# Kernel optimization log

Measured on AMD Instinct MI355X. Metric: run time of the kernel, lower is better.

## Reference

```python
import jax, jax.numpy as jnp
import numpy as np

HIDDEN = 2048
NUM_HEADS = 16
NUM_KV_HEADS = 8
HEAD_DIM = 128
EPS = 1e-6
ROPE_THETA = 10000.0
SEQ = 2048
Q_SIZE = NUM_HEADS * HEAD_DIM
KV_SIZE = NUM_KV_HEADS * HEAD_DIM


def rmsnorm_f32(x, w, eps=EPS):
    # RMSNormF32: normalize in float32, scale by weight
    xf = x.astype(jnp.float32)
    var = jnp.mean(xf * xf, axis=-1, keepdims=True)
    return xf * jax.lax.rsqrt(var + eps) * w.astype(jnp.float32)


def apply_rope(x, cos, sin):
    # x: [S, H, D]; cos/sin: [S, D//2] (neox-style half split)
    half = x.shape[-1] // 2
    x1, x2 = x[..., :half], x[..., half:]
    c = cos[:, None, :]
    s = sin[:, None, :]
    return jnp.concatenate([x1 * c - x2 * s, x2 * c + x1 * s], axis=-1)


def setup_inputs() -> dict:
    key = jax.random.key(0)
    ks = jax.random.split(key, 6)
    return {
        "positions": jnp.arange(SEQ, dtype=jnp.int32),
        "hidden_states": jax.random.normal(ks[0], (SEQ, HIDDEN), jnp.float32),
        "ln_weight": 1.0 + 0.1 * jax.random.normal(ks[1], (HIDDEN,), jnp.float32),
        "qkv_weight": 0.02 * jax.random.normal(ks[2], (Q_SIZE + 2 * KV_SIZE, HIDDEN), jnp.float32),
        "q_norm_weight": 1.0 + 0.1 * jax.random.normal(ks[3], (HEAD_DIM,), jnp.float32),
        "k_norm_weight": 1.0 + 0.1 * jax.random.normal(ks[4], (HEAD_DIM,), jnp.float32),
        "o_weight": 0.02 * jax.random.normal(ks[5], (HIDDEN, Q_SIZE), jnp.float32),
    }


def reference(positions, hidden_states, ln_weight, qkv_weight, q_norm_weight, k_norm_weight, o_weight):
    S = hidden_states.shape[0]
    # 1. input RMSNorm (f32)
    normalized = rmsnorm_f32(hidden_states, ln_weight)
    # 2. fused QKV projection (no bias)
    qkv = normalized @ qkv_weight.T  # [S, q_size + 2*kv_size]
    q = qkv[:, :Q_SIZE].reshape(S, NUM_HEADS, HEAD_DIM)
    k = qkv[:, Q_SIZE:Q_SIZE + KV_SIZE].reshape(S, NUM_KV_HEADS, HEAD_DIM)
    v = qkv[:, Q_SIZE + KV_SIZE:].reshape(S, NUM_KV_HEADS, HEAD_DIM)
    # 3. RoPE (neox half-split, cache built from theta)
    inv_freq = ROPE_THETA ** (-jnp.arange(0, HEAD_DIM, 2, dtype=jnp.float32) / HEAD_DIM)
    freqs = positions.astype(jnp.float32)[:, None] * inv_freq[None, :]  # [S, D/2]
    cos, sin = jnp.cos(freqs), jnp.sin(freqs)
    q = apply_rope(q, cos, sin)
    k = apply_rope(k, cos, sin)
    # 4. per-head q/k RMSNorm (applied after RoPE, as in source)
    q = rmsnorm_f32(q, q_norm_weight)
    k = rmsnorm_f32(k, k_norm_weight)
    # 5. GQA expand kv heads
    rep = NUM_HEADS // NUM_KV_HEADS
    k = jnp.repeat(k, rep, axis=1)  # [S, NH, D]
    v = jnp.repeat(v, rep, axis=1)
    # 6. naive causal attention
    scores = jnp.einsum('shd,thd->hst', q, k) / (HEAD_DIM ** 0.5)  # [NH, S, S]
    causal = jnp.triu(jnp.ones((S, S), dtype=bool), k=1)
    scores = jnp.where(causal[None, :, :], -jnp.inf, scores)
    attn = jax.nn.softmax(scores, axis=-1)
    attn = jnp.nan_to_num(attn, nan=0.0)
    out = jnp.einsum('hst,thd->shd', attn, v).reshape(S, Q_SIZE)
    # 7. output projection
    return out @ o_weight.T
```

## Files before the change

### kernel.cpp

```cpp
#include <hip/hip_runtime.h>
#include <hip/hip_bf16.h>
#include <stdint.h>

typedef unsigned short u16;
typedef __attribute__((ext_vector_type(4))) float f32x4;
typedef __attribute__((ext_vector_type(8))) __bf16 bf16x8;
typedef __attribute__((ext_vector_type(8))) unsigned short u16x8;
typedef __attribute__((ext_vector_type(4))) unsigned short u16x4;

#define SEQ 2048
#define HID 2048
#define HD  128

__device__ __forceinline__ float b2f(u16 v) {
    union { float f; unsigned u; } c; c.u = ((unsigned)v) << 16; return c.f;
}
__device__ __forceinline__ u16 f2b(float f) {
    union { float f; unsigned u; } c; c.f = f;
    unsigned r = c.u + 0x7fffu + ((c.u >> 16) & 1u);
    return (u16)(r >> 16);
}
__device__ __forceinline__ bf16x8 tob(u16x8 v) {
    union { u16x8 u; bf16x8 b; } c; c.u = v; return c.b;
}
__device__ __forceinline__ u16x8 ld8(const u16* p) { return *(const u16x8*)p; }

typedef const __attribute__((address_space(1))) unsigned int* gas_ptr;
typedef __attribute__((address_space(3))) unsigned int* las_ptr;
__device__ __forceinline__ void gld16(const void* g, void* l) {
    __builtin_amdgcn_global_load_lds((gas_ptr)g, (las_ptr)l, 16, 0, 0);
}

__global__ __launch_bounds__(256) void k_conv(const float* __restrict__ src,
                                              u16* __restrict__ dst) {
    const size_t i = ((size_t)blockIdx.x * 256 + threadIdx.x) * 8;
    f32x4 a = *(const f32x4*)(src + i);
    f32x4 b = *(const f32x4*)(src + i + 4);
    u16x8 o;
#pragma unroll
    for (int e = 0; e < 4; ++e) { o[e] = f2b(a[e]); o[e + 4] = f2b(b[e]); }
    *(u16x8*)(dst + i) = o;
}

__global__ __launch_bounds__(256) void k_rmsnorm(const float* __restrict__ x,
                                                 const float* __restrict__ w,
                                                 u16* __restrict__ o) {
    const int row = blockIdx.x, t = threadIdx.x;
    const float* xr = x + (size_t)row * HID + t * 8;
    f32x4 xa = *(const f32x4*)xr;
    f32x4 xb = *(const f32x4*)(xr + 4);
    float xf[8]; float ss = 0.f;
#pragma unroll
    for (int e = 0; e < 4; ++e) { xf[e] = xa[e]; xf[e + 4] = xb[e]; }
#pragma unroll
    for (int e = 0; e < 8; ++e) ss += xf[e] * xf[e];
#pragma unroll
    for (int m = 32; m; m >>= 1) ss += __shfl_xor(ss, m);
    __shared__ float red[4];
    if ((t & 63) == 0) red[t >> 6] = ss;
    __syncthreads();
    ss = red[0] + red[1] + red[2] + red[3];
    const float sc = rsqrtf(ss * (1.0f / HID) + 1e-6f);
    f32x4 wa = *(const f32x4*)(w + t * 8);
    f32x4 wb = *(const f32x4*)(w + t * 8 + 4);
    u16x8 ov;
#pragma unroll
    for (int e = 0; e < 4; ++e) {
        ov[e] = f2b(xf[e] * sc * wa[e]);
        ov[e + 4] = f2b(xf[e + 4] * sc * wb[e]);
    }
    *(u16x8*)(o + (size_t)row * HID + t * 8) = ov;
}

#define STAGE_G(buf, k0)                                                      \
    do {                                                                      \
        char* a0 = (char*)&As[buf][0][0] + wave * 1024;                       \
        char* a1 = (char*)&As[buf][1][0] + wave * 1024;                       \
        char* b0 = (char*)&Bs[buf][0][0] + wave * 1024;                       \
        char* b1 = (char*)&Bs[buf][1][0] + wave * 1024;                       \
        gld16(ga + (k0), a0);                                                 \
        gld16(ga + (k0) + rowskip, a0 + 4096);                                \
        gld16(ga + (k0) + 32, a1);                                            \
        gld16(ga + (k0) + 32 + rowskip, a1 + 4096);                           \
        gld16(gb + (k0), b0);                                                 \
        gld16(gb + (k0) + rowskip, b0 + 4096);                                \
        gld16(gb + (k0) + 32, b1);                                            \
        gld16(gb + (k0) + 32 + rowskip, b1 + 4096);                           \
    } while (0)

__global__ __launch_bounds__(256) void k_gemm_qkv(const u16* __restrict__ A,
                                                  const u16* __restrict__ B,
                                                  u16* __restrict__ qraw,
                                                  u16* __restrict__ kraw,
                                                  u16* __restrict__ vtr,
                                                  int K) {
    __shared__ u16 As[2][2][128 * 32];
    __shared__ u16 Bs[2][2][128 * 32];
    const int tid = threadIdx.x;
    const int wave = tid >> 6, lane = tid & 63, quad = lane >> 4, l16 = lane & 15;
    const int wm = wave >> 1, wn = wave & 1;
    const int sw = (l16 >> 1) & 3;
    const int m0 = blockIdx.x * 128, n0 = blockIdx.y * 128;
    f32x4 acc[4][4];
#pragma unroll
    for (int i = 0; i < 4; ++i)
#pragma unroll
        for (int j = 0; j < 4; ++j) acc[i][j] = (f32x4){0.f, 0.f, 0.f, 0.f};

    const int gchunk = (tid & 3) ^ ((tid >> 3) & 3);
    const u16* ga = A + (size_t)(m0 + (tid >> 2)) * K + gchunk * 8;
    const u16* gb = B + (size_t)(n0 + (tid >> 2)) * K + gchunk * 8;
    const size_t rowskip = (size_t)64 * K;

    STAGE_G(0, 0);
    const int nk = K >> 6;
    for (int t = 0; t < nk; ++t) {
        const int cur = t & 1;
        if (t + 1 < nk) {
            STAGE_G(cur ^ 1, (t + 1) * 64);
            asm volatile("s_waitcnt vmcnt(8)" ::: "memory");
        } else {
            asm volatile("s_waitcnt vmcnt(0)" ::: "memory");
        }
        __builtin_amdgcn_s_barrier();
        asm volatile("" ::: "memory");
#pragma unroll
        for (int h = 0; h < 2; ++h) {
            const u16* as = &As[cur][h][0];
            const u16* bs = &Bs[cur][h][0];
            bf16x8 af[4], bfr[4];
#pragma unroll
            for (int i = 0; i < 4; ++i)
                af[i] = tob(ld8(as + (wm * 64 + i * 16 + l16) * 32 + ((quad ^ sw) << 3)));
#pragma unroll
            for (int j = 0; j < 4; ++j)
                bfr[j] = tob(ld8(bs + (wn * 64 + j * 16 + l16) * 32 + ((quad ^ sw) << 3)));
#pragma unroll
            for (int i = 0; i < 4; ++i)
#pragma unroll
                for (int j = 0; j < 4; ++j)
                    acc[i][j] = __builtin_amdgcn_mfma_f32_16x16x32_bf16(af[i], bfr[j], acc[i][j], 0, 0, 0);
        }
        asm volatile("" ::: "memory");
        __builtin_amdgcn_s_barrier();
    }
#pragma unroll
    for (int i = 0; i < 4; ++i) {
        const int row = m0 + wm * 64 + i * 16 + quad * 4;
#pragma unroll
        for (int j = 0; j < 4; ++j) {
            const int col = n0 + wn * 64 + j * 16 + l16;
#pragma unroll
            for (int r = 0; r < 4; ++r) {
                const u16 val = f2b(acc[i][j][r]);
                const int s = row + r;
                if (col < 2048) {
                    const int head = col >> 7, d = col & 127;
                    qraw[((size_t)head * SEQ + s) * HD + d] = val;
                } else if (col < 3072) {
                    const int c = col - 2048, kv = c >> 7, d = c & 127;
                    kraw[((size_t)kv * SEQ + s) * HD + d] = val;
                } else {
                    const int c = col - 3072, kv = c >> 7, d = c & 127;
                    vtr[(size_t)kv * HD * SEQ + (size_t)d * SEQ + s] = val;
                }
            }
        }
    }
}

__global__ __launch_bounds__(256) void k_gemm_of(const u16* __restrict__ A,
                                                 const u16* __restrict__ B,
                                                 float* __restrict__ C,
                                                 int N, int K) {
    __shared__ u16 As[2][2][128 * 32];
    __shared__ u16 Bs[2][2][128 * 32];
    const int tid = threadIdx.x;
    const int wave = tid >> 6, lane = tid & 63, quad = lane >> 4, l16 = lane & 15;
    const int wm = wave >> 1, wn = wave & 1;
    const int sw = (l16 >> 1) & 3;
    const int m0 = blockIdx.x * 128, n0 = blockIdx.y * 128;
    f32x4 acc[4][4];
#pragma unroll
    for (int i = 0; i < 4; ++i)
#pragma unroll
        for (int j = 0; j < 4; ++j) acc[i][j] = (f32x4){0.f, 0.f, 0.f, 0.f};

    const int gchunk = (tid & 3) ^ ((tid >> 3) & 3);
    const u16* ga = A + (size_t)(m0 + (tid >> 2)) * K + gchunk * 8;
    const u16* gb = B + (size_t)(n0 + (tid >> 2)) * K + gchunk * 8;
    const size_t rowskip = (size_t)64 * K;

    STAGE_G(0, 0);
    const int nk = K >> 6;
    for (int t = 0; t < nk; ++t) {
        const int cur = t & 1;
        if (t + 1 < nk) {
            STAGE_G(cur ^ 1, (t + 1) * 64);
            asm volatile("s_waitcnt vmcnt(8)" ::: "memory");
        } else {
            asm volatile("s_waitcnt vmcnt(0)" ::: "memory");
        }
        __builtin_amdgcn_s_barrier();
        asm volatile("" ::: "memory");
#pragma unroll
        for (int h = 0; h < 2; ++h) {
            const u16* as = &As[cur][h][0];
            const u16* bs = &Bs[cur][h][0];
            bf16x8 af[4], bfr[4];
#pragma unroll
            for (int i = 0; i < 4; ++i)
                af[i] = tob(ld8(as + (wm * 64 + i * 16 + l16) * 32 + ((quad ^ sw) << 3)));
#pragma unroll
            for (int j = 0; j < 4; ++j)
                bfr[j] = tob(ld8(bs + (wn * 64 + j * 16 + l16) * 32 + ((quad ^ sw) << 3)));
#pragma unroll
            for (int i = 0; i < 4; ++i)
#pragma unroll
                for (int j = 0; j < 4; ++j)
                    acc[i][j] = __builtin_amdgcn_mfma_f32_16x16x32_bf16(af[i], bfr[j], acc[i][j], 0, 0, 0);
        }
        asm volatile("" ::: "memory");
        __builtin_amdgcn_s_barrier();
    }
#pragma unroll
    for (int i = 0; i < 4; ++i) {
        const int row = m0 + wm * 64 + i * 16 + quad * 4;
#pragma unroll
        for (int j = 0; j < 4; ++j) {
            const int col = n0 + wn * 64 + j * 16 + l16;
#pragma unroll
            for (int r = 0; r < 4; ++r)
                C[(size_t)(row + r) * N + col] = acc[i][j][r];
        }
    }
}

__global__ __launch_bounds__(256) void k_ropenorm(const int* __restrict__ pos,
                                                  const float* __restrict__ qw,
                                                  const float* __restrict__ kw,
                                                  u16* __restrict__ qraw,
                                                  u16* __restrict__ kraw) {
    const int s = blockIdx.x;
    const int h = blockIdx.y * 4 + (threadIdx.x >> 6);
    const int d = threadIdx.x & 63;
    const bool isq = h < 16;
    u16* row = isq ? (qraw + ((size_t)h * SEQ + s) * HD)
                   : (kraw + ((size_t)(h - 16) * SEQ + s) * HD);
    const float x1 = b2f(row[d]), x2 = b2f(row[d + 64]);
    const float p = (float)pos[s];
    const float inv = exp2f(-(float)d * (2.0f / 128.0f) * 13.287712379549449f);
    const float fr = p * inv;
    const float c = cosf(fr), sn = sinf(fr);
    const float o1 = x1 * c - x2 * sn;
    const float o2 = x2 * c + x1 * sn;
    float ss = o1 * o1 + o2 * o2;
#pragma unroll
    for (int m = 32; m; m >>= 1) ss += __shfl_xor(ss, m);
    const float sc = rsqrtf(ss * (1.0f / HD) + 1e-6f);
    const float* w = isq ? qw : kw;
    row[d] = f2b(o1 * sc * w[d]);
    row[d + 64] = f2b(o2 * sc * w[d + 64]);
}

__global__ __launch_bounds__(256) void k_attn(const u16* __restrict__ qh,
                                              const u16* __restrict__ kh,
                                              const u16* __restrict__ vt,
                                              u16* __restrict__ out) {
    const int tid = threadIdx.x;
    const int wave = tid >> 6, lane = tid & 63, quad = lane >> 4, l16 = lane & 15;
    const int head = blockIdx.y;
    const int bx = blockIdx.x;
    const int f = (bx & 1) ? 31 - (bx >> 1) : (bx >> 1);
    const int qt = (head < 8) ? f : 31 - f;
    const int kvh = head >> 1;
    const int q0 = qt * 64;

    __shared__ u16 Ks[2][64 * 128];
    __shared__ u16 Vts[2][128 * 64];
    __shared__ u16 Ps[4][16 * 64];

    const u16* qbase = qh + ((size_t)head * SEQ + q0 + wave * 16) * HD;
    bf16x8 aq[4];
#pragma unroll
    for (int kk = 0; kk < 4; ++kk)
        aq[kk] = tob(ld8(qbase + l16 * HD + kk * 32 + quad * 8));

    f32x4 acco[8];
#pragma unroll
    for (int j = 0; j < 8; ++j) acco[j] = (f32x4){0.f, 0.f, 0.f, 0.f};
    float lsum = 0.f;

    const float sc = 0.08838834764831845f;
    const u16* kbase = kh + (size_t)kvh * SEQ * HD;
    const u16* vbase = vt + (size_t)kvh * HD * SEQ;
    const int ntiles = qt + 1;
    u16* pw = &Ps[wave][0];
    const int qrow_g = q0 + wave * 16 + l16;

    const u16* kg0 = kbase + (size_t)tid * 8;
    const u16* vg0 = vbase + (size_t)(tid >> 3) * SEQ + (size_t)(tid & 7) * 8;
    int kst[4], vst[4];
#pragma unroll
    for (int r = 0; r < 4; ++r) {
        const int krow = r * 16 + (tid >> 4);
        kst[r] = krow * 128 + (((tid & 15) ^ (krow & 7)) << 3);
        const int vrow = r * 32 + (tid >> 3);
        vst[r] = vrow * 64 + (((tid & 7) ^ (vrow & 7)) << 3);
    }

    u16x8 kreg[4], vreg[4];
#pragma unroll
    for (int r = 0; r < 4; ++r) {
        kreg[r] = ld8(kg0 + (size_t)r * 2048);
        vreg[r] = ld8(vg0 + (size_t)r * 32 * SEQ);
    }
#pragma unroll
    for (int r = 0; r < 4; ++r) {
        *(u16x8*)(&Ks[0][0] + kst[r]) = kreg[r];
        *(u16x8*)(&Vts[0][0] + vst[r]) = vreg[r];
    }
    __syncthreads();

    for (int kt = 0; kt < ntiles; ++kt) {
        const int cur = kt & 1;
        const u16* ksc = &Ks[cur][0];
        const u16* vsc = &Vts[cur][0];

        if (kt + 1 < ntiles) {
            const size_t koff = (size_t)(kt + 1) * 64;
#pragma unroll
            for (int r = 0; r < 4; ++r) {
                kreg[r] = ld8(kg0 + koff * HD + (size_t)r * 2048);
                vreg[r] = ld8(vg0 + koff + (size_t)r * 32 * SEQ);
            }
        }

        f32x4 accs[4];
#pragma unroll
        for (int j = 0; j < 4; ++j) accs[j] = (f32x4){0.f, 0.f, 0.f, 0.f};
#pragma unroll
        for (int kk = 0; kk < 4; ++kk) {
#pragma unroll
            for (int j = 0; j < 4; ++j) {
                const int krow = j * 16 + l16;
                const bf16x8 bk = tob(ld8(ksc + krow * 128 + (((kk * 4 + quad) ^ (krow & 7)) << 3)));
                accs[j] = __builtin_amdgcn_mfma_f32_16x16x32_bf16(bk, aq[kk], accs[j], 0, 0, 0);
            }
        }

        const int k0 = kt * 64;
#pragma unroll
        for (int j = 0; j < 4; ++j) {
            u16x4 pk;
#pragma unroll
            for (int r = 0; r < 4; ++r) {
                const int kpos = k0 + j * 16 + quad * 4 + r;
                const float p = (kpos > qrow_g) ? 0.f : __expf(accs[j][r] * sc);
                lsum += p;
                pk[r] = f2b(p);
            }
            const int blk = (j * 2 + (quad >> 1)) ^ (l16 & 7);
            *(u16x4*)(pw + l16 * 64 + (blk << 3) + ((quad & 1) << 2)) = pk;
        }

        if (kt + 1 < ntiles) {
            u16* ksn = &Ks[1 - cur][0];
            u16* vsn = &Vts[1 - cur][0];
#pragma unroll
            for (int r = 0; r < 4; ++r) {
                *(u16x8*)(ksn + kst[r]) = kreg[r];
                *(u16x8*)(vsn + vst[r]) = vreg[r];
            }
        }

#pragma unroll
        for (int kk = 0; kk < 2; ++kk) {
            const bf16x8 ap = tob(ld8(pw + l16 * 64 + (((kk * 4 + quad) ^ (l16 & 7)) << 3)));
#pragma unroll
            for (int j = 0; j < 8; ++j) {
                const int vrow = j * 16 + l16;
                const bf16x8 bv = tob(ld8(vsc + vrow * 64 + (((kk * 4 + quad) ^ (vrow & 7)) << 3)));
                acco[j] = __builtin_amdgcn_mfma_f32_16x16x32_bf16(ap, bv, acco[j], 0, 0, 0);
            }
        }

        __syncthreads();
    }

    float v = lsum;
    v += __shfl_xor(v, 16);
    v += __shfl_xor(v, 32);
    f32x4 il;
#pragma unroll
    for (int r = 0; r < 4; ++r) il[r] = 1.0f / __shfl(v, quad * 4 + r);
    const int rowb = q0 + wave * 16 + quad * 4;
#pragma unroll
    for (int j = 0; j < 8; ++j) {
        const int col = head * HD + j * 16 + l16;
#pragma unroll
        for (int r = 0; r < 4; ++r)
            out[(size_t)(rowb + r) * 2048 + col] = f2b(acco[j][r] * il[r]);
    }
}

extern "C" void kernel_launch(void* const* d_in, const int* in_sizes, int n_in,
                              void* d_out, int out_size, void* d_ws, size_t ws_size,
                              hipStream_t stream) {
    const int*   positions = (const int*)d_in[0];
    const float* hidden   = (const float*)d_in[1];
    const float* lnw      = (const float*)d_in[2];
    const float* qkvw     = (const float*)d_in[3];
    const float* qnw      = (const float*)d_in[4];
    const float* knw      = (const float*)d_in[5];
    const float* ow       = (const float*)d_in[6];
    float* outp = (float*)d_out;

    char* ws = (char*)d_ws;
    const size_t MB = 1024ull * 1024ull;
    u16* normed = (u16*)(ws + 0 * MB);
    u16* qraw   = (u16*)(ws + 8 * MB);
    u16* kraw   = (u16*)(ws + 16 * MB);
    u16* vtr    = (u16*)(ws + 20 * MB);
    u16* qkvwb  = (u16*)(ws + 24 * MB);
    u16* owb    = (u16*)(ws + 0 * MB);
    u16* attno  = (u16*)(ws + 24 * MB);

    k_rmsnorm <<<SEQ, 256, 0, stream>>>(hidden, lnw, normed);
    k_conv    <<<4096, 256, 0, stream>>>(qkvw, qkvwb);
    k_gemm_qkv<<<dim3(16, 32), 256, 0, stream>>>(normed, qkvwb, qraw, kraw, vtr, HID);
    k_ropenorm<<<dim3(SEQ, 6), 256, 0, stream>>>(positions, qnw, knw, qraw, kraw);
    k_conv    <<<2048, 256, 0, stream>>>(ow, owb);
    k_attn    <<<dim3(32, 16), 256, 0, stream>>>(qraw, kraw, vtr, attno);
    k_gemm_of <<<dim3(16, 16), 256, 0, stream>>>(attno, owb, outp, HID, HID);
}
```

Before: 256.1 us.

## Split attention KV tiles across two wave groups with shared-memory reduction

```diff
diff --git a/kernel.cpp b/kernel.cpp
--- a/kernel.cpp
+++ b/kernel.cpp
@@ -263,12 +263,15 @@
     row[d + 64] = f2b(o2 * sc * w[d + 64]);
 }
 
-__global__ __launch_bounds__(256) void k_attn(const u16* __restrict__ qh,
-                                              const u16* __restrict__ kh,
-                                              const u16* __restrict__ vt,
-                                              u16* __restrict__ out) {
+__global__ __launch_bounds__(512, 4) void k_attn(const u16* __restrict__ qh,
+                                                 const u16* __restrict__ kh,
+                                                 const u16* __restrict__ vt,
+                                                 u16* __restrict__ out) {
     const int tid = threadIdx.x;
     const int wave = tid >> 6, lane = tid & 63, quad = lane >> 4, l16 = lane & 15;
+    const int gid = wave >> 2;
+    const int wv = wave & 3;
+    const int gtid = tid & 255;
     const int head = blockIdx.y;
     const int bx = blockIdx.x;
     const int f = (bx & 1) ? 31 - (bx >> 1) : (bx >> 1);
@@ -278,9 +281,9 @@
 
     __shared__ u16 Ks[2][64 * 128];
     __shared__ u16 Vts[2][128 * 64];
-    __shared__ u16 Ps[4][16 * 64];
-
-    const u16* qbase = qh + ((size_t)head * SEQ + q0 + wave * 16) * HD;
+    __shared__ u16 Ps[8][16 * 64];
+
+    const u16* qbase = qh + ((size_t)head * SEQ + q0 + wv * 16) * HD;
     bf16x8 aq[4];
 #pragma unroll
     for (int kk = 0; kk < 4; ++kk)
@@ -295,40 +298,46 @@
     const u16* kbase = kh + (size_t)kvh * SEQ * HD;
     const u16* vbase = vt + (size_t)kvh * HD * SEQ;
     const int ntiles = qt + 1;
+    const int niter = (ntiles + 1) >> 1;
     u16* pw = &Ps[wave][0];
-    const int qrow_g = q0 + wave * 16 + l16;
-
-    const u16* kg0 = kbase + (size_t)tid * 8;
-    const u16* vg0 = vbase + (size_t)(tid >> 3) * SEQ + (size_t)(tid & 7) * 8;
+    const int qrow_g = q0 + wv * 16 + l16;
+
+    const u16* kg0 = kbase + (size_t)gtid * 8;
+    const u16* vg0 = vbase + (size_t)(gtid >> 3) * SEQ + (size_t)(gtid & 7) * 8;
     int kst[4], vst[4];
 #pragma unroll
     for (int r = 0; r < 4; ++r) {
-        const int krow = r * 16 + (tid >> 4);
-        kst[r] = krow * 128 + (((tid & 15) ^ (krow & 7)) << 3);
-        const int vrow = r * 32 + (tid >> 3);
-        vst[r] = vrow * 64 + (((tid & 7) ^ (vrow & 7)) << 3);
-    }
+        const int krow = r * 16 + (gtid >> 4);
+        kst[r] = krow * 128 + (((gtid & 15) ^ (krow & 7)) << 3);
+        const int vrow = r * 32 + (gtid >> 3);
+        vst[r] = vrow * 64 + (((gtid & 7) ^ (vrow & 7)) << 3);
+    }
+    u16* ksg = &Ks[gid][0];
+    u16* vsg = &Vts[gid][0];
 
     u16x8 kreg[4], vreg[4];
-#pragma unroll
-    for (int r = 0; r < 4; ++r) {
-        kreg[r] = ld8(kg0 + (size_t)r * 2048);
-        vreg[r] = ld8(vg0 + (size_t)r * 32 * SEQ);
-    }
-#pragma unroll
-    for (int r = 0; r < 4; ++r) {
-        *(u16x8*)(&Ks[0][0] + kst[r]) = kreg[r];
-        *(u16x8*)(&Vts[0][0] + vst[r]) = vreg[r];
+    {
+        const size_t koff = (size_t)gid * 64;
+#pragma unroll
+        for (int r = 0; r < 4; ++r) {
+            kreg[r] = ld8(kg0 + koff * HD + (size_t)r * 2048);
+            vreg[r] = ld8(vg0 + koff + (size_t)r * 32 * SEQ);
+        }
+#pragma unroll
+        for (int r = 0; r < 4; ++r) {
+            *(u16x8*)(ksg + kst[r]) = kreg[r];
+            *(u16x8*)(vsg + vst[r]) = vreg[r];
+        }
     }
     __syncthreads();
 
-    for (int kt = 0; kt < ntiles; ++kt) {
-        const int cur = kt & 1;
-        const u16* ksc = &Ks[cur][0];
-        const u16* vsc = &Vts[cur][0];
-
-        if (kt + 1 < ntiles) {
-            const size_t koff = (size_t)(kt + 1) * 64;
+    for (int i = 0; i < niter; ++i) {
+        const int kt = 2 * i + gid;
+        const bool active = kt < ntiles;
+        const bool havenext = (kt + 2) < ntiles;
+
+        if (havenext) {
+            const size_t koff = (size_t)(kt + 2) * 64;
 #pragma unroll
             for (int r = 0; r < 4; ++r) {
                 kreg[r] = ld8(kg0 + koff * HD + (size_t)r * 2048);
@@ -336,71 +345,89 @@
             }
         }
 
-        f32x4 accs[4];
-#pragma unroll
-        for (int j = 0; j < 4; ++j) accs[j] = (f32x4){0.f, 0.f, 0.f, 0.f};
-#pragma unroll
-        for (int kk = 0; kk < 4; ++kk) {
+        if (active) {
+            f32x4 accs[4];
+#pragma unroll
+            for (int j = 0; j < 4; ++j) accs[j] = (f32x4){0.f, 0.f, 0.f, 0.f};
+#pragma unroll
+            for (int kk = 0; kk < 4; ++kk) {
+#pragma unroll
+                for (int j = 0; j < 4; ++j) {
+                    const int krow = j * 16 + l16;
+                    const bf16x8 bk = tob(ld8(ksg + krow * 128 + (((kk * 4 + quad) ^ (krow & 7)) << 3)));
+                    accs[j] = __builtin_amdgcn_mfma_f32_16x16x32_bf16(bk, aq[kk], accs[j], 0, 0, 0);
+                }
+            }
+
+            const int k0 = kt * 64;
 #pragma unroll
             for (int j = 0; j < 4; ++j) {
-                const int krow = j * 16 + l16;
-                const bf16x8 bk = tob(ld8(ksc + krow * 128 + (((kk * 4 + quad) ^ (krow & 7)) << 3)));
-                accs[j] = __builtin_amdgcn_mfma_f32_16x16x32_bf16(bk, aq[kk], accs[j], 0, 0, 0);
-            }
-        }
-
-        const int k0 = kt * 64;
-#pragma unroll
-        for (int j = 0; j < 4; ++j) {
-            u16x4 pk;
+                u16x4 pk;
+#pragma unroll
+                for (int r = 0; r < 4; ++r) {
+                    const int kpos = k0 + j * 16 + quad * 4 + r;
+                    const float p = (kpos > qrow_g) ? 0.f : __expf(accs[j][r] * sc);
+                    lsum += p;
+                    pk[r] = f2b(p);
+                }
+                const int blk = (j * 2 + (quad >> 1)) ^ (l16 & 7);
+                *(u16x4*)(pw + l16 * 64 + (blk << 3) + ((quad & 1) << 2)) = pk;
+            }
+
+#pragma unroll
+            for (int kk = 0; kk < 2; ++kk) {
+                const bf16x8 ap = tob(ld8(pw + l16 * 64 + (((kk * 4 + quad) ^ (l16 & 7)) << 3)));
+#pragma unroll
+                for (int j = 0; j < 8; ++j) {
+                    const int vrow = j * 16 + l16;
+                    const bf16x8 bv = tob(ld8(vsg + vrow * 64 + (((kk * 4 + quad) ^ (vrow & 7)) << 3)));
+                    acco[j] = __builtin_amdgcn_mfma_f32_16x16x32_bf16(ap, bv, acco[j], 0, 0, 0);
+                }
+            }
+        }
+
+        __syncthreads();
+        if (havenext) {
 #pragma unroll
             for (int r = 0; r < 4; ++r) {
-                const int kpos = k0 + j * 16 + quad * 4 + r;
-                const float p = (kpos > qrow_g) ? 0.f : __expf(accs[j][r] * sc);
-                lsum += p;
-                pk[r] = f2b(p);
-            }
-            const int blk = (j * 2 + (quad >> 1)) ^ (l16 & 7);
-            *(u16x4*)(pw + l16 * 64 + (blk << 3) + ((quad & 1) << 2)) = pk;
-        }
-
-        if (kt + 1 < ntiles) {
-            u16* ksn = &Ks[1 - cur][0];
-            u16* vsn = &Vts[1 - cur][0];
-#pragma unroll
-            for (int r = 0; r < 4; ++r) {
-                *(u16x8*)(ksn + kst[r]) = kreg[r];
-                *(u16x8*)(vsn + vst[r]) = vreg[r];
-            }
-        }
-
-#pragma unroll
-        for (int kk = 0; kk < 2; ++kk) {
-            const bf16x8 ap = tob(ld8(pw + l16 * 64 + (((kk * 4 + quad) ^ (l16 & 7)) << 3)));
-#pragma unroll
-            for (int j = 0; j < 8; ++j) {
-                const int vrow = j * 16 + l16;
-                const bf16x8 bv = tob(ld8(vsc + vrow * 64 + (((kk * 4 + quad) ^ (vrow & 7)) << 3)));
-                acco[j] = __builtin_amdgcn_mfma_f32_16x16x32_bf16(ap, bv, acco[j], 0, 0, 0);
-            }
-        }
-
+                *(u16x8*)(ksg + kst[r]) = kreg[r];
+                *(u16x8*)(vsg + vst[r]) = vreg[r];
+            }
+        }
         __syncthreads();
     }
 
-    float v = lsum;
-    v += __shfl_xor(v, 16);
-    v += __shfl_xor(v, 32);
-    f32x4 il;
-#pragma unroll
-    for (int r = 0; r < 4; ++r) il[r] = 1.0f / __shfl(v, quad * 4 + r);
-    const int rowb = q0 + wave * 16 + quad * 4;
-#pragma unroll
-    for (int j = 0; j < 8; ++j) {
-        const int col = head * HD + j * 16 + l16;
-#pragma unroll
-        for (int r = 0; r < 4; ++r)
-            out[(size_t)(rowb + r) * 2048 + col] = f2b(acco[j][r] * il[r]);
+    float* mo = (float*)&Ks[0][0];
+    float* ml = (float*)&Vts[0][0];
+    if (gid == 1) {
+#pragma unroll
+        for (int j = 0; j < 8; ++j)
+            *(f32x4*)(mo + (size_t)wv * 2048 + lane * 32 + ((j ^ (lane & 7)) << 2)) = acco[j];
+        ml[wv * 64 + lane] = lsum;
+    }
+    __syncthreads();
+    if (gid == 0) {
+#pragma unroll
+        for (int j = 0; j < 8; ++j) {
+            const f32x4 p = *(const f32x4*)(mo + (size_t)wv * 2048 + lane * 32 + ((j ^ (lane & 7)) << 2));
+            acco[j] += p;
+        }
+        lsum += ml[wv * 64 + lane];
+
+        float v = lsum;
+        v += __shfl_xor(v, 16);
+        v += __shfl_xor(v, 32);
+        f32x4 il;
+#pragma unroll
+        for (int r = 0; r < 4; ++r) il[r] = 1.0f / __shfl(v, quad * 4 + r);
+        const int rowb = q0 + wv * 16 + quad * 4;
+#pragma unroll
+        for (int j = 0; j < 8; ++j) {
+            const int col = head * HD + j * 16 + l16;
+#pragma unroll
+            for (int r = 0; r < 4; ++r)
+                out[(size_t)(rowb + r) * 2048 + col] = f2b(acco[j][r] * il[r]);
+        }
     }
 }
 
@@ -431,6 +458,6 @@
     k_gemm_qkv<<<dim3(16, 32), 256, 0, stream>>>(normed, qkvwb, qraw, kraw, vtr, HID);
     k_ropenorm<<<dim3(SEQ, 6), 256, 0, stream>>>(positions, qnw, knw, qraw, kraw);
     k_conv    <<<2048, 256, 0, stream>>>(ow, owb);
-    k_attn    <<<dim3(32, 16), 256, 0, stream>>>(qraw, kraw, vtr, attno);
+    k_attn    <<<dim3(32, 16), 512, 0, stream>>>(qraw, kraw, vtr, attno);
     k_gemm_of <<<dim3(16, 16), 256, 0, stream>>>(attno, owb, outp, HID, HID);
 }
```

After: 255.8 us. Within noise of the previous version (-0.1%).

## Restructure attention so each wave owns a 32-row slice and reads K/V directly

Applied to the files above, without the earlier changes.

```diff
diff --git a/kernel.cpp b/kernel.cpp
--- a/kernel.cpp
+++ b/kernel.cpp
@@ -263,144 +263,127 @@
     row[d + 64] = f2b(o2 * sc * w[d + 64]);
 }
 
-__global__ __launch_bounds__(256) void k_attn(const u16* __restrict__ qh,
-                                              const u16* __restrict__ kh,
-                                              const u16* __restrict__ vt,
-                                              u16* __restrict__ out) {
+__global__ __launch_bounds__(256, 1) void k_attn(const u16* __restrict__ qh,
+                                                 const u16* __restrict__ kh,
+                                                 const u16* __restrict__ vt,
+                                                 u16* __restrict__ out) {
     const int tid = threadIdx.x;
     const int wave = tid >> 6, lane = tid & 63, quad = lane >> 4, l16 = lane & 15;
-    const int head = blockIdx.y;
-    const int bx = blockIdx.x;
-    const int f = (bx & 1) ? 31 - (bx >> 1) : (bx >> 1);
-    const int qt = (head < 8) ? f : 31 - f;
-    const int kvh = head >> 1;
-    const int q0 = qt * 64;
-
-    __shared__ u16 Ks[2][64 * 128];
-    __shared__ u16 Vts[2][128 * 64];
-    __shared__ u16 Ps[4][16 * 64];
-
-    const u16* qbase = qh + ((size_t)head * SEQ + q0 + wave * 16) * HD;
-    bf16x8 aq[4];
-#pragma unroll
-    for (int kk = 0; kk < 4; ++kk)
-        aq[kk] = tob(ld8(qbase + l16 * HD + kk * 32 + quad * 8));
-
-    f32x4 acco[8];
-#pragma unroll
-    for (int j = 0; j < 8; ++j) acco[j] = (f32x4){0.f, 0.f, 0.f, 0.f};
-    float lsum = 0.f;
+    const int b = blockIdx.x;
+    const int kvh = b & 7;
+    const int j5 = b >> 3;
+    const int head = kvh * 2 + (j5 & 1);
+    const int p = j5 >> 1;
+    const int slice = (wave & 1) ? ((wave & 2) ? 63 : 31) - p
+                                 : ((wave & 2) ? 32 : 0) + p;
+    const int s0 = slice * 32;
+    const int nt = (s0 >> 6) + 1;
+
+    __shared__ u16 Ps[4][2][16 * 64];
+
+    const u16* qbase = qh + ((size_t)head * SEQ + s0) * HD;
+    bf16x8 aq[2][4];
+#pragma unroll
+    for (int u = 0; u < 2; ++u)
+#pragma unroll
+        for (int kk = 0; kk < 4; ++kk)
+            aq[u][kk] = tob(ld8(qbase + (u * 16 + l16) * HD + kk * 32 + quad * 8));
+
+    f32x4 acco[2][8];
+#pragma unroll
+    for (int u = 0; u < 2; ++u)
+#pragma unroll
+        for (int j = 0; j < 8; ++j) acco[u][j] = (f32x4){0.f, 0.f, 0.f, 0.f};
+    float lsum[2] = {0.f, 0.f};
 
     const float sc = 0.08838834764831845f;
     const u16* kbase = kh + (size_t)kvh * SEQ * HD;
     const u16* vbase = vt + (size_t)kvh * HD * SEQ;
-    const int ntiles = qt + 1;
-    u16* pw = &Ps[wave][0];
-    const int qrow_g = q0 + wave * 16 + l16;
-
-    const u16* kg0 = kbase + (size_t)tid * 8;
-    const u16* vg0 = vbase + (size_t)(tid >> 3) * SEQ + (size_t)(tid & 7) * 8;
-    int kst[4], vst[4];
-#pragma unroll
-    for (int r = 0; r < 4; ++r) {
-        const int krow = r * 16 + (tid >> 4);
-        kst[r] = krow * 128 + (((tid & 15) ^ (krow & 7)) << 3);
-        const int vrow = r * 32 + (tid >> 3);
-        vst[r] = vrow * 64 + (((tid & 7) ^ (vrow & 7)) << 3);
-    }
-
-    u16x8 kreg[4], vreg[4];
-#pragma unroll
-    for (int r = 0; r < 4; ++r) {
-        kreg[r] = ld8(kg0 + (size_t)r * 2048);
-        vreg[r] = ld8(vg0 + (size_t)r * 32 * SEQ);
-    }
-#pragma unroll
-    for (int r = 0; r < 4; ++r) {
-        *(u16x8*)(&Ks[0][0] + kst[r]) = kreg[r];
-        *(u16x8*)(&Vts[0][0] + vst[r]) = vreg[r];
-    }
-    __syncthreads();
-
-    for (int kt = 0; kt < ntiles; ++kt) {
-        const int cur = kt & 1;
-        const u16* ksc = &Ks[cur][0];
-        const u16* vsc = &Vts[cur][0];
-
-        if (kt + 1 < ntiles) {
-            const size_t koff = (size_t)(kt + 1) * 64;
-#pragma unroll
-            for (int r = 0; r < 4; ++r) {
-                kreg[r] = ld8(kg0 + koff * HD + (size_t)r * 2048);
-                vreg[r] = ld8(vg0 + koff + (size_t)r * 32 * SEQ);
+    const int qrow0 = s0 + l16;
+
+    for (int kt = 0; kt < nt; ++kt) {
+        const int k0 = kt * 64;
+
+        u16x8 kreg[16];
+#pragma unroll
+        for (int kk = 0; kk < 4; ++kk)
+#pragma unroll
+            for (int j = 0; j < 4; ++j)
+                kreg[kk * 4 + j] = ld8(kbase + (size_t)(k0 + j * 16 + l16) * HD + kk * 32 + quad * 8);
+
+        f32x4 accs[2][4];
+#pragma unroll
+        for (int u = 0; u < 2; ++u)
+#pragma unroll
+            for (int j = 0; j < 4; ++j) accs[u][j] = (f32x4){0.f, 0.f, 0.f, 0.f};
+#pragma unroll
+        for (int kk = 0; kk < 4; ++kk)
+#pragma unroll
+            for (int j = 0; j < 4; ++j) {
+                const bf16x8 bk = tob(kreg[kk * 4 + j]);
+#pragma unroll
+                for (int u = 0; u < 2; ++u)
+                    accs[u][j] = __builtin_amdgcn_mfma_f32_16x16x32_bf16(bk, aq[u][kk], accs[u][j], 0, 0, 0);
             }
-        }
-
-        f32x4 accs[4];
-#pragma unroll
-        for (int j = 0; j < 4; ++j) accs[j] = (f32x4){0.f, 0.f, 0.f, 0.f};
-#pragma unroll
-        for (int kk = 0; kk < 4; ++kk) {
+
+        u16x8 vreg[16];
+#pragma unroll
+        for (int kk = 0; kk < 2; ++kk)
+#pragma unroll
+            for (int j = 0; j < 8; ++j)
+                vreg[kk * 8 + j] = ld8(vbase + (size_t)(j * 16 + l16) * SEQ + k0 + kk * 32 + quad * 8);
+
+#pragma unroll
+        for (int u = 0; u < 2; ++u) {
+            u16* pwu = &Ps[wave][u][0];
+            const int qrg = qrow0 + u * 16;
 #pragma unroll
             for (int j = 0; j < 4; ++j) {
-                const int krow = j * 16 + l16;
-                const bf16x8 bk = tob(ld8(ksc + krow * 128 + (((kk * 4 + quad) ^ (krow & 7)) << 3)));
-                accs[j] = __builtin_amdgcn_mfma_f32_16x16x32_bf16(bk, aq[kk], accs[j], 0, 0, 0);
+                u16x4 pk;
+#pragma unroll
+                for (int r = 0; r < 4; ++r) {
+                    const int kpos = k0 + j * 16 + quad * 4 + r;
+                    const float pv = (kpos > qrg) ? 0.f : __expf(accs[u][j][r] * sc);
+                    lsum[u] += pv;
+                    pk[r] = f2b(pv);
+                }
+                const int blk = (j * 2 + (quad >> 1)) ^ (l16 & 7);
+                *(u16x4*)(pwu + l16 * 64 + (blk << 3) + ((quad & 1) << 2)) = pk;
             }
         }
 
-        const int k0 = kt * 64;
-#pragma unroll
-        for (int j = 0; j < 4; ++j) {
-            u16x4 pk;
-#pragma unroll
-            for (int r = 0; r < 4; ++r) {
-                const int kpos = k0 + j * 16 + quad * 4 + r;
-                const float p = (kpos > qrow_g) ? 0.f : __expf(accs[j][r] * sc);
-                lsum += p;
-                pk[r] = f2b(p);
+#pragma unroll
+        for (int kk = 0; kk < 2; ++kk) {
+            bf16x8 ap[2];
+#pragma unroll
+            for (int u = 0; u < 2; ++u)
+                ap[u] = tob(ld8(&Ps[wave][u][0] + l16 * 64 + (((kk * 4 + quad) ^ (l16 & 7)) << 3)));
+#pragma unroll
+            for (int j = 0; j < 8; ++j) {
+                const bf16x8 bv = tob(vreg[kk * 8 + j]);
+#pragma unroll
+                for (int u = 0; u < 2; ++u)
+                    acco[u][j] = __builtin_amdgcn_mfma_f32_16x16x32_bf16(ap[u], bv, acco[u][j], 0, 0, 0);
             }
-            const int blk = (j * 2 + (quad >> 1)) ^ (l16 & 7);
-            *(u16x4*)(pw + l16 * 64 + (blk << 3) + ((quad & 1) << 2)) = pk;
-        }
-
-        if (kt + 1 < ntiles) {
-            u16* ksn = &Ks[1 - cur][0];
-            u16* vsn = &Vts[1 - cur][0];
-#pragma unroll
-            for (int r = 0; r < 4; ++r) {
-                *(u16x8*)(ksn + kst[r]) = kreg[r];
-                *(u16x8*)(vsn + vst[r]) = vreg[r];
-            }
-        }
-
-#pragma unroll
-        for (int kk = 0; kk < 2; ++kk) {
-            const bf16x8 ap = tob(ld8(pw + l16 * 64 + (((kk * 4 + quad) ^ (l16 & 7)) << 3)));
-#pragma unroll
-            for (int j = 0; j < 8; ++j) {
-                const int vrow = j * 16 + l16;
-                const bf16x8 bv = tob(ld8(vsc + vrow * 64 + (((kk * 4 + quad) ^ (vrow & 7)) << 3)));
-                acco[j] = __builtin_amdgcn_mfma_f32_16x16x32_bf16(ap, bv, acco[j], 0, 0, 0);
-            }
-        }
-
-        __syncthreads();
-    }
-
-    float v = lsum;
-    v += __shfl_xor(v, 16);
-    v += __shfl_xor(v, 32);
-    f32x4 il;
-#pragma unroll
-    for (int r = 0; r < 4; ++r) il[r] = 1.0f / __shfl(v, quad * 4 + r);
-    const int rowb = q0 + wave * 16 + quad * 4;
-#pragma unroll
-    for (int j = 0; j < 8; ++j) {
-        const int col = head * HD + j * 16 + l16;
-#pragma unroll
-        for (int r = 0; r < 4; ++r)
-            out[(size_t)(rowb + r) * 2048 + col] = f2b(acco[j][r] * il[r]);
+        }
+    }
+
+#pragma unroll
+    for (int u = 0; u < 2; ++u) {
+        float v = lsum[u];
+        v += __shfl_xor(v, 16);
+        v += __shfl_xor(v, 32);
+        f32x4 il;
+#pragma unroll
+        for (int r = 0; r < 4; ++r) il[r] = 1.0f / __shfl(v, quad * 4 + r);
+        const int rowb = s0 + u * 16 + quad * 4;
+#pragma unroll
+        for (int j = 0; j < 8; ++j) {
+            const int col = head * HD + j * 16 + l16;
+#pragma unroll
+            for (int r = 0; r < 4; ++r)
+                out[(size_t)(rowb + r) * 2048 + col] = f2b(acco[u][j][r] * il[r]);
+        }
     }
 }
 
@@ -431,6 +414,6 @@
     k_gemm_qkv<<<dim3(16, 32), 256, 0, stream>>>(normed, qkvwb, qraw, kraw, vtr, HID);
     k_ropenorm<<<dim3(SEQ, 6), 256, 0, stream>>>(positions, qnw, knw, qraw, kraw);
     k_conv    <<<2048, 256, 0, stream>>>(ow, owb);
-    k_attn    <<<dim3(32, 16), 256, 0, stream>>>(qraw, kraw, vtr, attno);
+    k_attn    <<<dim3(256), 256, 0, stream>>>(qraw, kraw, vtr, attno);
     k_gemm_of <<<dim3(16, 16), 256, 0, stream>>>(attno, owb, outp, HID, HID);
 }
```

Result: slower. 327.0 us (+27.7%).

## Split long causal attention query tiles across KV partitions with merge kernel

Applied to the files above, without the earlier changes.

```diff
diff --git a/kernel.cpp b/kernel.cpp
--- a/kernel.cpp
+++ b/kernel.cpp
@@ -263,21 +263,26 @@
     row[d + 64] = f2b(o2 * sc * w[d + 64]);
 }
 
-__global__ __launch_bounds__(256) void k_attn(const u16* __restrict__ qh,
-                                              const u16* __restrict__ kh,
-                                              const u16* __restrict__ vt,
-                                              u16* __restrict__ out) {
+__global__ __launch_bounds__(256, 4) void k_attn(const u16* __restrict__ qh,
+                                                 const u16* __restrict__ kh,
+                                                 const u16* __restrict__ vt,
+                                                 u16* __restrict__ out,
+                                                 u16* __restrict__ po,
+                                                 float* __restrict__ pl) {
     const int tid = threadIdx.x;
     const int wave = tid >> 6, lane = tid & 63, quad = lane >> 4, l16 = lane & 15;
     const int head = blockIdx.y;
-    const int bx = blockIdx.x;
-    const int f = (bx & 1) ? 31 - (bx >> 1) : (bx >> 1);
-    const int qt = (head < 8) ? f : 31 - f;
+    const int b = blockIdx.x;
+    int qt, part, np;
+    if (b < 11)      { qt = b;                      part = 0;            np = 1; }
+    else if (b < 33) { qt = 11 + ((b - 11) >> 1);   part = (b - 11) & 1; np = 2; }
+    else             { qt = 22 + (b - 33) / 3;      part = (b - 33) % 3; np = 3; }
     const int kvh = head >> 1;
     const int q0 = qt * 64;
-
-    __shared__ u16 Ks[2][64 * 128];
-    __shared__ u16 Vts[2][128 * 64];
+    const int ntiles = qt + 1;
+
+    __shared__ u16 Ks[64 * 128];
+    __shared__ u16 Vts[128 * 64];
     __shared__ u16 Ps[4][16 * 64];
 
     const u16* qbase = qh + ((size_t)head * SEQ + q0 + wave * 16) * HD;
@@ -294,7 +299,6 @@
     const float sc = 0.08838834764831845f;
     const u16* kbase = kh + (size_t)kvh * SEQ * HD;
     const u16* vbase = vt + (size_t)kvh * HD * SEQ;
-    const int ntiles = qt + 1;
     u16* pw = &Ps[wave][0];
     const int qrow_g = q0 + wave * 16 + l16;
 
@@ -310,25 +314,25 @@
     }
 
     u16x8 kreg[4], vreg[4];
-#pragma unroll
-    for (int r = 0; r < 4; ++r) {
-        kreg[r] = ld8(kg0 + (size_t)r * 2048);
-        vreg[r] = ld8(vg0 + (size_t)r * 32 * SEQ);
-    }
-#pragma unroll
-    for (int r = 0; r < 4; ++r) {
-        *(u16x8*)(&Ks[0][0] + kst[r]) = kreg[r];
-        *(u16x8*)(&Vts[0][0] + vst[r]) = vreg[r];
+    {
+        const size_t koff = (size_t)part * 64;
+#pragma unroll
+        for (int r = 0; r < 4; ++r) {
+            kreg[r] = ld8(kg0 + koff * HD + (size_t)r * 2048);
+            vreg[r] = ld8(vg0 + koff + (size_t)r * 32 * SEQ);
+        }
+#pragma unroll
+        for (int r = 0; r < 4; ++r) {
+            *(u16x8*)(&Ks[0] + kst[r]) = kreg[r];
+            *(u16x8*)(&Vts[0] + vst[r]) = vreg[r];
+        }
     }
     __syncthreads();
 
-    for (int kt = 0; kt < ntiles; ++kt) {
-        const int cur = kt & 1;
-        const u16* ksc = &Ks[cur][0];
-        const u16* vsc = &Vts[cur][0];
-
-        if (kt + 1 < ntiles) {
-            const size_t koff = (size_t)(kt + 1) * 64;
+    for (int kt = part; kt < ntiles; kt += np) {
+        const bool havenext = (kt + np) < ntiles;
+        if (havenext) {
+            const size_t koff = (size_t)(kt + np) * 64;
 #pragma unroll
             for (int r = 0; r < 4; ++r) {
                 kreg[r] = ld8(kg0 + koff * HD + (size_t)r * 2048);
@@ -344,7 +348,7 @@
 #pragma unroll
             for (int j = 0; j < 4; ++j) {
                 const int krow = j * 16 + l16;
-                const bf16x8 bk = tob(ld8(ksc + krow * 128 + (((kk * 4 + quad) ^ (krow & 7)) << 3)));
+                const bf16x8 bk = tob(ld8(&Ks[0] + krow * 128 + (((kk * 4 + quad) ^ (krow & 7)) << 3)));
                 accs[j] = __builtin_amdgcn_mfma_f32_16x16x32_bf16(bk, aq[kk], accs[j], 0, 0, 0);
             }
         }
@@ -356,52 +360,94 @@
 #pragma unroll
             for (int r = 0; r < 4; ++r) {
                 const int kpos = k0 + j * 16 + quad * 4 + r;
-                const float p = (kpos > qrow_g) ? 0.f : __expf(accs[j][r] * sc);
-                lsum += p;
-                pk[r] = f2b(p);
+                const float pv = (kpos > qrow_g) ? 0.f : __expf(accs[j][r] * sc);
+                lsum += pv;
+                pk[r] = f2b(pv);
             }
             const int blk = (j * 2 + (quad >> 1)) ^ (l16 & 7);
             *(u16x4*)(pw + l16 * 64 + (blk << 3) + ((quad & 1) << 2)) = pk;
         }
 
-        if (kt + 1 < ntiles) {
-            u16* ksn = &Ks[1 - cur][0];
-            u16* vsn = &Vts[1 - cur][0];
-#pragma unroll
-            for (int r = 0; r < 4; ++r) {
-                *(u16x8*)(ksn + kst[r]) = kreg[r];
-                *(u16x8*)(vsn + vst[r]) = vreg[r];
-            }
-        }
-
 #pragma unroll
         for (int kk = 0; kk < 2; ++kk) {
             const bf16x8 ap = tob(ld8(pw + l16 * 64 + (((kk * 4 + quad) ^ (l16 & 7)) << 3)));
 #pragma unroll
             for (int j = 0; j < 8; ++j) {
                 const int vrow = j * 16 + l16;
-                const bf16x8 bv = tob(ld8(vsc + vrow * 64 + (((kk * 4 + quad) ^ (vrow & 7)) << 3)));
+                const bf16x8 bv = tob(ld8(&Vts[0] + vrow * 64 + (((kk * 4 + quad) ^ (vrow & 7)) << 3)));
                 acco[j] = __builtin_amdgcn_mfma_f32_16x16x32_bf16(ap, bv, acco[j], 0, 0, 0);
             }
         }
 
+        __syncthreads();
+        if (havenext) {
+#pragma unroll
+            for (int r = 0; r < 4; ++r) {
+                *(u16x8*)(&Ks[0] + kst[r]) = kreg[r];
+                *(u16x8*)(&Vts[0] + vst[r]) = vreg[r];
+            }
+        }
         __syncthreads();
     }
 
     float v = lsum;
     v += __shfl_xor(v, 16);
     v += __shfl_xor(v, 32);
-    f32x4 il;
-#pragma unroll
-    for (int r = 0; r < 4; ++r) il[r] = 1.0f / __shfl(v, quad * 4 + r);
     const int rowb = q0 + wave * 16 + quad * 4;
-#pragma unroll
-    for (int j = 0; j < 8; ++j) {
-        const int col = head * HD + j * 16 + l16;
-#pragma unroll
-        for (int r = 0; r < 4; ++r)
-            out[(size_t)(rowb + r) * 2048 + col] = f2b(acco[j][r] * il[r]);
-    }
+
+    if (np == 1) {
+        f32x4 il;
+#pragma unroll
+        for (int r = 0; r < 4; ++r) il[r] = 1.0f / __shfl(v, quad * 4 + r);
+#pragma unroll
+        for (int j = 0; j < 8; ++j) {
+            const int col = head * HD + j * 16 + l16;
+#pragma unroll
+            for (int r = 0; r < 4; ++r)
+                out[(size_t)(rowb + r) * 2048 + col] = f2b(acco[j][r] * il[r]);
+        }
+    } else {
+        u16* pob = po + (size_t)part * SEQ * 2048;
+        float* plb = pl + (size_t)part * 16 * SEQ;
+        if (lane < 16) plb[head * SEQ + q0 + wave * 16 + l16] = v;
+#pragma unroll
+        for (int j = 0; j < 8; ++j) {
+            const int col = head * HD + j * 16 + l16;
+#pragma unroll
+            for (int r = 0; r < 4; ++r)
+                pob[(size_t)(rowb + r) * 2048 + col] = f2b(acco[j][r]);
+        }
+    }
+}
+
+__global__ __launch_bounds__(256) void k_amerge(const u16* __restrict__ po,
+                                                const float* __restrict__ pl,
+                                                u16* __restrict__ out) {
+    const int s = blockIdx.x + 704;
+    const int qt = s >> 6;
+    const int np = (qt > 21) ? 3 : 2;
+    const int t = threadIdx.x;
+    const int head = t >> 4;
+
+    float l = 0.f;
+#pragma unroll
+    for (int p = 0; p < 3; ++p)
+        if (p < np) l += pl[(size_t)p * 16 * SEQ + head * SEQ + s];
+    const float il = 1.0f / l;
+
+    float o[8] = {0.f, 0.f, 0.f, 0.f, 0.f, 0.f, 0.f, 0.f};
+#pragma unroll
+    for (int p = 0; p < 3; ++p) {
+        if (p < np) {
+            const u16x8 vv = ld8(po + (size_t)p * SEQ * 2048 + (size_t)s * 2048 + t * 8);
+#pragma unroll
+            for (int e = 0; e < 8; ++e) o[e] += b2f(vv[e]);
+        }
+    }
+    u16x8 ov;
+#pragma unroll
+    for (int e = 0; e < 8; ++e) ov[e] = f2b(o[e] * il);
+    *(u16x8*)(out + (size_t)s * 2048 + t * 8) = ov;
 }
 
 extern "C" void kernel_launch(void* const* d_in, const int* in_sizes, int n_in,
@@ -425,12 +471,15 @@
     u16* qkvwb  = (u16*)(ws + 24 * MB);
     u16* owb    = (u16*)(ws + 0 * MB);
     u16* attno  = (u16*)(ws + 24 * MB);
+    u16* po     = (u16*)(ws + 32 * MB);
+    float* pl   = (float*)(ws + 56 * MB);
 
     k_rmsnorm <<<SEQ, 256, 0, stream>>>(hidden, lnw, normed);
     k_conv    <<<4096, 256, 0, stream>>>(qkvw, qkvwb);
     k_gemm_qkv<<<dim3(16, 32), 256, 0, stream>>>(normed, qkvwb, qraw, kraw, vtr, HID);
     k_ropenorm<<<dim3(SEQ, 6), 256, 0, stream>>>(positions, qnw, knw, qraw, kraw);
     k_conv    <<<2048, 256, 0, stream>>>(ow, owb);
-    k_attn    <<<dim3(32, 16), 256, 0, stream>>>(qraw, kraw, vtr, attno);
+    k_attn    <<<dim3(63, 16), 256, 0, stream>>>(qraw, kraw, vtr, attno, po, pl);
+    k_amerge  <<<1344, 256, 0, stream>>>(po, pl, attno);
     k_gemm_of <<<dim3(16, 16), 256, 0, stream>>>(attno, owb, outp, HID, HID);
 }
```

After: 254.3 us. About the same (-0.7%).
